# Performance work log

Measured on AMD Instinct MI355X. Metric: run time of the kernel, lower is better.

## Reference

```python
import jax, jax.numpy as jnp
import numpy as np

B, C, H, W = 2, 512, 64, 64
G = 32          # GroupNorm groups
EPS = 1e-6


def setup_inputs() -> dict:
    key = jax.random.key(0)
    ks = jax.random.split(key, 10)
    s = 1.0 / np.sqrt(C)
    return {
        "x": jax.random.normal(ks[0], (B, C, H, W), dtype=jnp.float32),
        "gn_w": jnp.ones((C,), jnp.float32),
        "gn_b": jnp.zeros((C,), jnp.float32),
        "wq": jax.random.normal(ks[1], (C, C), jnp.float32) * s,
        "bq": jnp.zeros((C,), jnp.float32),
        "wk": jax.random.normal(ks[2], (C, C), jnp.float32) * s,
        "bk": jnp.zeros((C,), jnp.float32),
        "wv": jax.random.normal(ks[3], (C, C), jnp.float32) * s,
        "bv": jnp.zeros((C,), jnp.float32),
        "wo": jax.random.normal(ks[4], (C, C), jnp.float32) * s,
        "bo": jnp.zeros((C,), jnp.float32),
    }


def reference(x, gn_w, gn_b, wq, bq, wk, bk, wv, bv, wo, bo):
    b, c, h, w = x.shape
    n = h * w
    # GroupNorm(32, eps=1e-6, affine)
    xg = x.reshape(b, G, c // G, h, w)
    mu = xg.mean(axis=(2, 3, 4), keepdims=True)
    var = ((xg - mu) ** 2).mean(axis=(2, 3, 4), keepdims=True)
    hn = ((xg - mu) * jax.lax.rsqrt(var + EPS)).reshape(b, c, h, w)
    hn = hn * gn_w[None, :, None, None] + gn_b[None, :, None, None]
    # 1x1 convs == per-pixel linear over channels; tokens: b n c
    hf = hn.reshape(b, c, n)
    q = jnp.einsum('oc,bcn->bno', wq, hf) + bq  # [b, n, c]
    k = jnp.einsum('oc,bcn->bno', wk, hf) + bk
    v = jnp.einsum('oc,bcn->bno', wv, hf) + bv
    scale = jnp.asarray(c, x.dtype) ** -0.5
    att = jax.nn.softmax(jnp.einsum('bic,bjc->bij', q, k) * scale, axis=-1)
    o = jnp.einsum('bij,bjc->bic', att, v)      # [b, n, c]
    out = jnp.einsum('oc,bnc->bno', wo, o) + bo # proj_out
    return x + out.transpose(0, 2, 1).reshape(b, c, h, w)
```

## Files before the change

kernel.cpp:

```cpp
#include <hip/hip_runtime.h>
#include <hip/hip_bf16.h>


typedef float f32x4 __attribute__((ext_vector_type(4)));
typedef __bf16 bf16x8 __attribute__((ext_vector_type(8)));

typedef const __attribute__((address_space(1))) unsigned char* gas_p;
typedef __attribute__((address_space(3))) unsigned char* las_p;

__device__ __forceinline__ void gload_lds16(const void* g, void* l) {
  __builtin_amdgcn_global_load_lds((gas_p)g, (las_p)l, 16, 0, 0);
}

__global__ __launch_bounds__(256) void prelude_k(
    const float* __restrict__ wq, const float* __restrict__ wk,
    const float* __restrict__ wv, const float* __restrict__ wo,
    __hip_bfloat16* __restrict__ wqkb, __hip_bfloat16* __restrict__ wvb,
    __hip_bfloat16* __restrict__ wob, const float* __restrict__ bq,
    const float* __restrict__ bk, float* __restrict__ bqk,
    const float* __restrict__ x, float* __restrict__ stats) {
  int bid = blockIdx.x;
  if (bid < 4096) {
    const float* src;
    __hip_bfloat16* dst;
    if (bid < 1024)      { src = wq; dst = wqkb; }
    else if (bid < 2048) { src = wk; dst = wqkb + 262144; }
    else if (bid < 3072) { src = wv; dst = wvb; }
    else                 { src = wo; dst = wob; }
    int i = (bid & 1023) * 256 + threadIdx.x;
    dst[i] = __float2bfloat16(src[i]);
    return;
  }
  if (bid < 4160) {
    int bg = bid - 4096;
    const float4* p = (const float4*)(x + (size_t)bg * 65536);
    float s = 0.f, s2 = 0.f;
    for (int i = threadIdx.x; i < 16384; i += 256) {
      float4 v = p[i];
      s  += v.x + v.y + v.z + v.w;
      s2 += v.x * v.x + v.y * v.y + v.z * v.z + v.w * v.w;
    }
#pragma unroll
    for (int off = 32; off > 0; off >>= 1) {
      s  += __shfl_xor(s, off);
      s2 += __shfl_xor(s2, off);
    }
    __shared__ float rs[4], rs2[4];
    int wid = threadIdx.x >> 6, lane = threadIdx.x & 63;
    if (lane == 0) { rs[wid] = s; rs2[wid] = s2; }
    __syncthreads();
    if (threadIdx.x == 0) {
      float S  = rs[0] + rs[1] + rs[2] + rs[3];
      float S2 = rs2[0] + rs2[1] + rs2[2] + rs2[3];
      float mean = S * (1.f / 65536.f);
      float var  = S2 * (1.f / 65536.f) - mean * mean;
      stats[bg * 2]     = mean;
      stats[bg * 2 + 1] = rsqrtf(var + 1e-6f);
    }
    return;
  }
  for (int j = threadIdx.x; j < 1024; j += 256)
    bqk[j] = (j < 512) ? bq[j] : bk[j - 512];
}

__global__ __launch_bounds__(256) void gn_apply_k(const float* __restrict__ x,
                                                  const float* __restrict__ stats,
                                                  const float* __restrict__ gw,
                                                  const float* __restrict__ gb,
                                                  __hip_bfloat16* __restrict__ hf) {
  int c0 = blockIdx.x * 64, n0 = blockIdx.y * 64, b = blockIdx.z;
  __shared__ float tile[64][65];
  int tid = threadIdx.x;
  int cl = tid >> 2, q = tid & 3;
  int c = c0 + cl;
  float mean = stats[(b * 32 + (c >> 4)) * 2];
  float rstd = stats[(b * 32 + (c >> 4)) * 2 + 1];
  float sc = rstd * gw[c];
  float sh = gb[c] - mean * sc;
  const float* xr = x + ((size_t)(b * 512 + c0 + cl)) * 4096 + n0 + q * 16;
#pragma unroll
  for (int j = 0; j < 4; j++) {
    float4 v = *(const float4*)(xr + 4 * j);
    int n = q * 16 + 4 * j;
    tile[cl][n]     = v.x * sc + sh;
    tile[cl][n + 1] = v.y * sc + sh;
    tile[cl][n + 2] = v.z * sc + sh;
    tile[cl][n + 3] = v.w * sc + sh;
  }
  __syncthreads();
  int nl = tid >> 2, ch = q * 16;
  bf16x8 o0, o1;
#pragma unroll
  for (int l = 0; l < 8; l++) {
    o0[l] = (__bf16)tile[ch + l][nl];
    o1[l] = (__bf16)tile[ch + 8 + l][nl];
  }
  __hip_bfloat16* op = hf + ((size_t)(b * 4096 + n0 + nl)) * 512 + c0 + ch;
  *(uint4*)op = *(uint4*)&o0;
  *(uint4*)(op + 8) = *(uint4*)&o1;
}

__global__ __launch_bounds__(256, 4) void qkv_k(
    const __hip_bfloat16* __restrict__ hf, const __hip_bfloat16* __restrict__ wqk,
    const __hip_bfloat16* __restrict__ wv, const float* __restrict__ bqk,
    const float* __restrict__ bv, __hip_bfloat16* __restrict__ qk,
    __hip_bfloat16* __restrict__ vT) {
  bool isV = blockIdx.x >= 8;
  int m0 = isV ? (blockIdx.x - 8) * 128 : blockIdx.y * 128;
  int n0 = isV ? blockIdx.y * 128 : blockIdx.x * 128;
  const __hip_bfloat16* A  = isV ? wv : hf;
  const __hip_bfloat16* Bm = isV ? hf : wqk;

  __shared__ __align__(16) unsigned char smem[34816];
  __hip_bfloat16* As  = (__hip_bfloat16*)smem;
  __hip_bfloat16* Bs  = As + 8192;
  __hip_bfloat16* epi = (__hip_bfloat16*)smem;

  int tid  = threadIdx.x;
  int wvx  = tid >> 6, lane = tid & 63;
  int wr   = (wvx >> 1) * 64, wc = (wvx & 1) * 64;
  int quad = lane >> 4, l16 = lane & 15;

  int srow = wvx * 32 + (lane >> 2);
  int scol = (lane & 3) * 8;
  const __hip_bfloat16* gA0 = A  + (size_t)(m0 + srow) * 512 + scol;
  const __hip_bfloat16* gA1 = gA0 + (size_t)16 * 512;
  const __hip_bfloat16* gB0 = Bm + (size_t)(n0 + srow) * 512 + scol;
  const __hip_bfloat16* gB1 = gB0 + (size_t)16 * 512;

  auto stage = [&](int kk, int bsel) {
    int lb = bsel * 4096 + wvx * 1024;
    gload_lds16(gA0 + kk, &As[lb]);
    gload_lds16(gA1 + kk, &As[lb + 512]);
    gload_lds16(gB0 + kk, &Bs[lb]);
    gload_lds16(gB1 + kk, &Bs[lb + 512]);
  };

  f32x4 acc[4][4] = {};
  stage(0, 0);
  for (int kt = 0; kt < 16; kt++) {
    __syncthreads();
    if (kt + 1 < 16) stage((kt + 1) << 5, (kt + 1) & 1);
    const __hip_bfloat16* Ab = &As[(kt & 1) * 4096];
    const __hip_bfloat16* Bb = &Bs[(kt & 1) * 4096];
    bf16x8 af[4], bfr[4];
#pragma unroll
    for (int i = 0; i < 4; i++)
      af[i] = *(const bf16x8*)&Ab[(wr + i * 16 + l16) * 32 + quad * 8];
#pragma unroll
    for (int j = 0; j < 4; j++)
      bfr[j] = *(const bf16x8*)&Bb[(wc + j * 16 + l16) * 32 + quad * 8];
#pragma unroll
    for (int i = 0; i < 4; i++)
#pragma unroll
      for (int j = 0; j < 4; j++)
        acc[i][j] = __builtin_amdgcn_mfma_f32_16x16x32_bf16(af[i], bfr[j],
                                                            acc[i][j], 0, 0, 0);
  }

  float bj[4], bm[4][4];
  if (!isV) {
#pragma unroll
    for (int j = 0; j < 4; j++) bj[j] = bqk[n0 + wc + j * 16 + l16];
  } else {
#pragma unroll
    for (int i = 0; i < 4; i++)
#pragma unroll
      for (int r = 0; r < 4; r++)
        bm[i][r] = bv[m0 + wr + i * 16 + quad * 4 + r];
  }
  __syncthreads();
#pragma unroll
  for (int i = 0; i < 4; i++)
#pragma unroll
    for (int j = 0; j < 4; j++)
#pragma unroll
      for (int r = 0; r < 4; r++) {
        int ml = wr + i * 16 + quad * 4 + r;
        int nl = wc + j * 16 + l16;
        float v = acc[i][j][r] + (isV ? bm[i][r] : bj[j]);
        epi[ml * 136 + nl] = __float2bfloat16(v);
      }
  __syncthreads();
  int mr = tid >> 1, h = tid & 1;
  const __hip_bfloat16* rowp = &epi[mr * 136 + h * 64];
  if (!isV) {
    __hip_bfloat16* o = qk + (size_t)(m0 + mr) * 1024 + n0 + h * 64;
#pragma unroll
    for (int c = 0; c < 8; c++)
      *(uint4*)(o + c * 8) = *(const uint4*)(rowp + c * 8);
  } else {
    int b = (n0 + h * 64) >> 12, t = (n0 + h * 64) & 4095;
    __hip_bfloat16* o = vT + ((size_t)(b * 512 + m0 + mr)) * 4096 + t;
#pragma unroll
    for (int c = 0; c < 8; c++)
      *(uint4*)(o + c * 8) = *(const uint4*)(rowp + c * 8);
  }
}

__global__ __launch_bounds__(512, 4) void attn_k(
    const __hip_bfloat16* __restrict__ qk, const __hip_bfloat16* __restrict__ vT,
    __hip_bfloat16* __restrict__ part, float* __restrict__ rsum) {
  const float scale = 0.044194173824159216f;
  int bid = blockIdx.x;
  int g = bid & 7;
  int b = g >> 2, spl = g & 3;
  int qtile = bid >> 3;

  const __hip_bfloat16* qkb = qk + (size_t)b * 4194304;
  const __hip_bfloat16* vTb = vT + (size_t)b * 2097152;

  __shared__ __align__(16) unsigned char smem[74752];
  __hip_bfloat16* Qs = (__hip_bfloat16*)smem;
  __hip_bfloat16* Ps = (__hip_bfloat16*)(smem + 65536);
  float* Rs = (float*)(smem + 73728);

  int tid = threadIdx.x, wv = tid >> 6, lane = tid & 63;
  int quad = lane >> 4, l16 = lane & 15;
  int kvc0 = wv * 16;

  __hip_bfloat16* slot = (__hip_bfloat16*)(smem + 32768 + wv * 4096);

#pragma unroll
  for (int i = 0; i < 4; i++) {
    int r = wv * 4 + i;
    gload_lds16(qkb + (size_t)(qtile * 32 + r) * 1024 + (lane ^ (r & 7)) * 8,
                &Qs[r * 512]);
  }

  const __hip_bfloat16* gKw =
      qkb + (size_t)(spl * 1024 + wv * 16 + (lane >> 2)) * 1024 + 512 +
      ((lane & 3) ^ ((lane >> 2) & 3)) * 8;
  auto stageK32 = [&](int t, int s) {
    gload_lds16(gKw + (size_t)t * 131072 + s * 32, slot + (s & 3) * 512);
  };

  const __hip_bfloat16* gVw =
      vTb + (size_t)(wv * 64 + (lane >> 2)) * 4096 + spl * 1024 +
      ((lane & 3) ^ ((lane >> 2) & 3)) * 8;
  auto stageVp = [&](int t, int sub) {
#pragma unroll
    for (int c = 0; c < 4; c++)
      gload_lds16(gVw + (size_t)t * 128 + sub * 32 + (size_t)(c * 16) * 4096,
                  slot + c * 512);
  };

  f32x4 accS[2] = {};
  f32x4 accO[2][4] = {};
  float rsr[8] = {};

  stageK32(0, 0);
  stageK32(0, 1);
  stageK32(0, 2);
  asm volatile("s_waitcnt vmcnt(3)" ::: "memory");
  __builtin_amdgcn_s_barrier();
  asm volatile("" ::: "memory");

  for (int t = 0; t < 8; t++) {
#pragma unroll
    for (int s = 0; s < 16; s++) {
      if (s < 13) {
        stageK32(t, s + 3);
        asm volatile("s_waitcnt vmcnt(3)" ::: "memory");
      } else if (s == 13) {
        asm volatile("s_waitcnt vmcnt(2)" ::: "memory");
      } else if (s == 14) {
        asm volatile("s_waitcnt vmcnt(1)" ::: "memory");
      } else {
        asm volatile("s_waitcnt vmcnt(0)" ::: "memory");
      }
      const __hip_bfloat16* Kb = slot + (s & 3) * 512;
      int rk = kvc0 + l16;
      (void)rk;
      bf16x8 bk = *(const bf16x8*)&Kb[l16 * 32 + ((quad ^ (l16 & 3)) << 3)];
#pragma unroll
      for (int qg = 0; qg < 2; qg++) {
        int rq = qg * 16 + l16;
        bf16x8 aq = *(const bf16x8*)
            &Qs[rq * 512 + (((s * 4 + quad) ^ (rq & 7)) << 3)];
        accS[qg] = __builtin_amdgcn_mfma_f32_16x16x32_bf16(aq, bk, accS[qg],
                                                           0, 0, 0);
      }
    }
    asm volatile("s_waitcnt lgkmcnt(0)" ::: "memory");
    stageVp(t, 0);
#pragma unroll
    for (int qg = 0; qg < 2; qg++) {
#pragma unroll
      for (int rr = 0; rr < 4; rr++) {
        float p = __expf(accS[qg][rr] * scale);
        rsr[qg * 4 + rr] += p;
        int row = qg * 16 + quad * 4 + rr;
        int col = kvc0 + l16;
        Ps[row * 128 + (((col >> 3) ^ (row & 7)) << 3) + (col & 7)] =
            __float2bfloat16(p);
      }
      accS[qg] = (f32x4){0.f, 0.f, 0.f, 0.f};
    }
    asm volatile("s_waitcnt lgkmcnt(0)" ::: "memory");
    __builtin_amdgcn_s_barrier();
    asm volatile("" ::: "memory");
#pragma unroll
    for (int sub = 0; sub < 4; sub++) {
      asm volatile("s_waitcnt vmcnt(0)" ::: "memory");
      bf16x8 pa[2], bvf[4];
#pragma unroll
      for (int qg = 0; qg < 2; qg++) {
        int rq = qg * 16 + l16;
        pa[qg] = *(const bf16x8*)
            &Ps[rq * 128 + (((sub * 4 + quad) ^ (rq & 7)) << 3)];
      }
#pragma unroll
      for (int dj = 0; dj < 4; dj++)
        bvf[dj] = *(const bf16x8*)
            &slot[(dj * 16 + l16) * 32 + ((quad ^ (l16 & 3)) << 3)];
      asm volatile("s_waitcnt lgkmcnt(0)" ::: "memory");
      __builtin_amdgcn_sched_barrier(0);
      if (sub < 3) stageVp(t, sub + 1);
#pragma unroll
      for (int dj = 0; dj < 4; dj++)
#pragma unroll
        for (int qg = 0; qg < 2; qg++)
          accO[qg][dj] = __builtin_amdgcn_mfma_f32_16x16x32_bf16(
              pa[qg], bvf[dj], accO[qg][dj], 0, 0, 0);
    }
    asm volatile("" ::: "memory");
    __builtin_amdgcn_s_barrier();
    asm volatile("" ::: "memory");
    if (t + 1 < 8) {
      stageK32(t + 1, 0);
      stageK32(t + 1, 1);
      stageK32(t + 1, 2);
    }
  }

  size_t pbase = ((size_t)(spl * 2 + b) * 4096 + qtile * 32) * 512;
#pragma unroll
  for (int qg = 0; qg < 2; qg++)
#pragma unroll
    for (int rr = 0; rr < 4; rr++) {
      int row = qg * 16 + quad * 4 + rr;
#pragma unroll
      for (int dj = 0; dj < 4; dj++)
        part[pbase + (size_t)row * 512 + wv * 64 + dj * 16 + l16] =
            __float2bfloat16(accO[qg][dj][rr]);
    }
#pragma unroll
  for (int k = 0; k < 8; k++)
#pragma unroll
    for (int off = 1; off < 16; off <<= 1) rsr[k] += __shfl_xor(rsr[k], off);
  if (l16 == 0) {
#pragma unroll
    for (int qg = 0; qg < 2; qg++)
#pragma unroll
      for (int rr = 0; rr < 4; rr++)
        Rs[wv * 32 + qg * 16 + quad * 4 + rr] = rsr[qg * 4 + rr];
  }
  __syncthreads();
  if (tid < 32) {
    float s = 0.f;
#pragma unroll
    for (int w = 0; w < 8; w++) s += Rs[w * 32 + tid];
    rsum[spl * 8192 + b * 4096 + qtile * 32 + tid] = s;
  }
}

__global__ __launch_bounds__(256) void reduce2_k(
    const __hip_bfloat16* __restrict__ part, const float* __restrict__ rsum,
    __hip_bfloat16* __restrict__ obuf) {
  size_t i8 = (size_t)blockIdx.x * 256 + threadIdx.x;
  size_t perb = 262144;
  size_t b = i8 / perb, r = i8 - b * perb;
  int t = (int)(r >> 6);
  float ps = rsum[b * 4096 + t] + rsum[8192 + b * 4096 + t] +
             rsum[16384 + b * 4096 + t] + rsum[24576 + b * 4096 + t];
  float inv = 1.f / ps;
  float acc[8] = {};
#pragma unroll
  for (int sp = 0; sp < 4; sp++) {
    bf16x8 v = ((const bf16x8*)part)[(sp * 2 + b) * perb + r];
#pragma unroll
    for (int l = 0; l < 8; l++) acc[l] += (float)v[l];
  }
  bf16x8 o;
#pragma unroll
  for (int l = 0; l < 8; l++) o[l] = (__bf16)(acc[l] * inv);
  ((bf16x8*)obuf)[b * perb + r] = o;
}

__global__ __launch_bounds__(256, 2) void oproj_k(
    const __hip_bfloat16* __restrict__ Wo, const __hip_bfloat16* __restrict__ O,
    float* __restrict__ out, const float* __restrict__ bias,
    const float* __restrict__ resid) {
  int m0 = blockIdx.y * 64, n0 = blockIdx.x * 128, bb = blockIdx.z;
  O += (size_t)bb * 4096 * 512;
  size_t cbase = (size_t)bb * 512 * 4096;

  __shared__ __align__(16) unsigned char smem[24576];
  __hip_bfloat16* As  = (__hip_bfloat16*)smem;
  __hip_bfloat16* Bs  = As + 4096;
  __hip_bfloat16* epi = (__hip_bfloat16*)smem;

  int tid = threadIdx.x, wv = tid >> 6, lane = tid & 63;
  int wr = (wv >> 1) * 32, wc = (wv & 1) * 64;
  int quad = lane >> 4, l16 = lane & 15;

  int lr = lane >> 2, scol = (lane & 3) * 8;
  const __hip_bfloat16* gA  = Wo + (size_t)(m0 + wv * 16 + lr) * 512 + scol;
  const __hip_bfloat16* gB0 = O  + (size_t)(n0 + wv * 32 + lr) * 512 + scol;
  const __hip_bfloat16* gB1 = gB0 + (size_t)16 * 512;

  auto stage = [&](int kk, int bsel) {
    gload_lds16(gA + kk, &As[bsel * 2048 + wv * 512]);
    gload_lds16(gB0 + kk, &Bs[bsel * 4096 + wv * 1024]);
    gload_lds16(gB1 + kk, &Bs[bsel * 4096 + wv * 1024 + 512]);
  };

  f32x4 acc[2][4] = {};
  stage(0, 0);
  for (int kt = 0; kt < 16; kt++) {
    __syncthreads();
    if (kt + 1 < 16) stage((kt + 1) << 5, (kt + 1) & 1);
    const __hip_bfloat16* Ab = &As[(kt & 1) * 2048];
    const __hip_bfloat16* Bb = &Bs[(kt & 1) * 4096];
    bf16x8 af[2], bfr[4];
#pragma unroll
    for (int i = 0; i < 2; i++)
      af[i] = *(const bf16x8*)&Ab[(wr + i * 16 + l16) * 32 + quad * 8];
#pragma unroll
    for (int j = 0; j < 4; j++)
      bfr[j] = *(const bf16x8*)&Bb[(wc + j * 16 + l16) * 32 + quad * 8];
#pragma unroll
    for (int i = 0; i < 2; i++)
#pragma unroll
      for (int j = 0; j < 4; j++)
        acc[i][j] = __builtin_amdgcn_mfma_f32_16x16x32_bf16(af[i], bfr[j],
                                                            acc[i][j], 0, 0, 0);
  }

  float pre[2][4];
#pragma unroll
  for (int i = 0; i < 2; i++)
#pragma unroll
    for (int r = 0; r < 4; r++)
      pre[i][r] = bias[m0 + wr + i * 16 + quad * 4 + r];
  __syncthreads();
#pragma unroll
  for (int i = 0; i < 2; i++)
#pragma unroll
    for (int j = 0; j < 4; j++)
#pragma unroll
      for (int r = 0; r < 4; r++)
        epi[(wr + i * 16 + quad * 4 + r) * 136 + wc + j * 16 + l16] =
            __float2bfloat16(acc[i][j][r] + pre[i][r]);
  __syncthreads();
  int mr = tid >> 2, seg = tid & 3;
  const __hip_bfloat16* rowp = &epi[mr * 136 + seg * 32];
  size_t obase = cbase + (size_t)(m0 + mr) * 4096 + n0 + seg * 32;
#pragma unroll
  for (int c = 0; c < 4; c++) {
    bf16x8 val = *(const bf16x8*)(rowp + c * 8);
    size_t idx = obase + c * 8;
    float4 r0 = *(const float4*)&resid[idx];
    float4 r1 = *(const float4*)&resid[idx + 4];
    float4 o0, o1;
    o0.x = r0.x + (float)val[0]; o0.y = r0.y + (float)val[1];
    o0.z = r0.z + (float)val[2]; o0.w = r0.w + (float)val[3];
    o1.x = r1.x + (float)val[4]; o1.y = r1.y + (float)val[5];
    o1.z = r1.z + (float)val[6]; o1.w = r1.w + (float)val[7];
    *(float4*)&out[idx] = o0;
    *(float4*)&out[idx + 4] = o1;
  }
}

extern "C" void kernel_launch(void* const* d_in, const int* in_sizes, int n_in,
                              void* d_out, int out_size, void* d_ws,
                              size_t ws_size, hipStream_t stream) {
  const float* xp  = (const float*)d_in[0];
  const float* gwp = (const float*)d_in[1];
  const float* gbp = (const float*)d_in[2];
  const float* wqp = (const float*)d_in[3];
  const float* bqp = (const float*)d_in[4];
  const float* wkp = (const float*)d_in[5];
  const float* bkp = (const float*)d_in[6];
  const float* wvp = (const float*)d_in[7];
  const float* bvp = (const float*)d_in[8];
  const float* wop = (const float*)d_in[9];
  const float* bop = (const float*)d_in[10];
  float* outp = (float*)d_out;

  char* w = (char*)d_ws;
  size_t off = 0;
  auto alloc = [&](size_t bytes) {
    void* p = w + off;
    off += (bytes + 255) & ~(size_t)255;
    return p;
  };
  float* stats         = (float*)alloc(64 * 2 * sizeof(float));
  __hip_bfloat16* hf   = (__hip_bfloat16*)alloc((size_t)2 * 4096 * 512 * 2);
  __hip_bfloat16* wqkb = (__hip_bfloat16*)alloc((size_t)1024 * 512 * 2);
  __hip_bfloat16* wvb  = (__hip_bfloat16*)alloc((size_t)512 * 512 * 2);
  __hip_bfloat16* wob  = (__hip_bfloat16*)alloc((size_t)512 * 512 * 2);
  float* bqk           = (float*)alloc(1024 * sizeof(float));
  float* rsum          = (float*)alloc((size_t)4 * 2 * 4096 * sizeof(float));
  __hip_bfloat16* qk   = (__hip_bfloat16*)alloc((size_t)2 * 4096 * 1024 * 2);
  __hip_bfloat16* vT   = (__hip_bfloat16*)alloc((size_t)2 * 512 * 4096 * 2);
  __hip_bfloat16* obuf = (__hip_bfloat16*)alloc((size_t)2 * 4096 * 512 * 2);
  __hip_bfloat16* part = (__hip_bfloat16*)alloc((size_t)8 * 4096 * 512 * 2);

  prelude_k<<<4161, 256, 0, stream>>>(wqp, wkp, wvp, wop, wqkb, wvb, wob,
                                      bqp, bkp, bqk, xp, stats);

  gn_apply_k<<<dim3(8, 64, 2), 256, 0, stream>>>(xp, stats, gwp, gbp, hf);

  qkv_k<<<dim3(12, 64, 1), 256, 0, stream>>>(hf, wqkb, wvb, bqk, bvp, qk, vT);

  attn_k<<<1024, 512, 0, stream>>>(qk, vT, part, rsum);

  reduce2_k<<<2048, 256, 0, stream>>>(part, rsum, obuf);

  oproj_k<<<dim3(32, 8, 2), 256, 0, stream>>>(wob, obuf, outp, bop, xp);
}
```

Baseline: 284.2 us.

## Hold Q fragments in registers, deepen K staging, double-buffer V tiles

```diff
diff --git a/kernel.cpp b/kernel.cpp
--- a/kernel.cpp
+++ b/kernel.cpp
@@ -198,7 +198,7 @@
   }
 }
 
-__global__ __launch_bounds__(512, 4) void attn_k(
+__global__ __launch_bounds__(512, 2) void attn_k(
     const __hip_bfloat16* __restrict__ qk, const __hip_bfloat16* __restrict__ vT,
     __hip_bfloat16* __restrict__ part, float* __restrict__ rsum) {
   const float scale = 0.044194173824159216f;
@@ -210,99 +210,111 @@
   const __hip_bfloat16* qkb = qk + (size_t)b * 4194304;
   const __hip_bfloat16* vTb = vT + (size_t)b * 2097152;
 
-  __shared__ __align__(16) unsigned char smem[74752];
-  __hip_bfloat16* Qs = (__hip_bfloat16*)smem;
-  __hip_bfloat16* Ps = (__hip_bfloat16*)(smem + 65536);
-  float* Rs = (float*)(smem + 73728);
+  __shared__ __align__(16) unsigned char smem[140288];
+  __hip_bfloat16* Ps = (__hip_bfloat16*)smem;
+  float* Rs = (float*)(smem + 139264);
 
   int tid = threadIdx.x, wv = tid >> 6, lane = tid & 63;
   int quad = lane >> 4, l16 = lane & 15;
   int kvc0 = wv * 16;
 
-  __hip_bfloat16* slot = (__hip_bfloat16*)(smem + 32768 + wv * 4096);
-
-#pragma unroll
-  for (int i = 0; i < 4; i++) {
-    int r = wv * 4 + i;
-    gload_lds16(qkb + (size_t)(qtile * 32 + r) * 1024 + (lane ^ (r & 7)) * 8,
-                &Qs[r * 512]);
+  __hip_bfloat16* slot = (__hip_bfloat16*)(smem + 8192 + wv * 16384);
+
+  bf16x8 qfrag[2][16];
+  {
+    const __hip_bfloat16* qrow0 =
+        qkb + (size_t)(qtile * 32 + l16) * 1024 + quad * 8;
+    const __hip_bfloat16* qrow1 = qrow0 + (size_t)16 * 1024;
+#pragma unroll
+    for (int s = 0; s < 16; s++) qfrag[0][s] = *(const bf16x8*)(qrow0 + s * 32);
+#pragma unroll
+    for (int s = 0; s < 16; s++) qfrag[1][s] = *(const bf16x8*)(qrow1 + s * 32);
   }
 
   const __hip_bfloat16* gKw =
       qkb + (size_t)(spl * 1024 + wv * 16 + (lane >> 2)) * 1024 + 512 +
       ((lane & 3) ^ ((lane >> 2) & 3)) * 8;
-  auto stageK32 = [&](int t, int s) {
-    gload_lds16(gKw + (size_t)t * 131072 + s * 32, slot + (s & 3) * 512);
+  auto stageK = [&](int t, int s) {
+    gload_lds16(gKw + (size_t)t * 131072 + s * 32, slot + s * 512);
   };
 
   const __hip_bfloat16* gVw =
       vTb + (size_t)(wv * 64 + (lane >> 2)) * 4096 + spl * 1024 +
       ((lane & 3) ^ ((lane >> 2) & 3)) * 8;
-  auto stageVp = [&](int t, int sub) {
+  auto stageV = [&](int t, int sub, int h) {
 #pragma unroll
     for (int c = 0; c < 4; c++)
       gload_lds16(gVw + (size_t)t * 128 + sub * 32 + (size_t)(c * 16) * 4096,
-                  slot + c * 512);
+                  slot + 4096 + h * 2048 + c * 512);
   };
 
   f32x4 accS[2] = {};
   f32x4 accO[2][4] = {};
-  float rsr[8] = {};
-
-  stageK32(0, 0);
-  stageK32(0, 1);
-  stageK32(0, 2);
-  asm volatile("s_waitcnt vmcnt(3)" ::: "memory");
-  __builtin_amdgcn_s_barrier();
-  asm volatile("" ::: "memory");
+  float rsr[2] = {};
+
+#pragma unroll
+  for (int p = 0; p < 8; p++) stageK(0, p);
 
   for (int t = 0; t < 8; t++) {
 #pragma unroll
     for (int s = 0; s < 16; s++) {
-      if (s < 13) {
-        stageK32(t, s + 3);
-        asm volatile("s_waitcnt vmcnt(3)" ::: "memory");
-      } else if (s == 13) {
-        asm volatile("s_waitcnt vmcnt(2)" ::: "memory");
-      } else if (s == 14) {
-        asm volatile("s_waitcnt vmcnt(1)" ::: "memory");
+      if (s < 8) {
+        stageK(t, s + 8);
+        asm volatile("s_waitcnt vmcnt(8)" ::: "memory");
+      } else if (s == 8)  asm volatile("s_waitcnt vmcnt(7)" ::: "memory");
+      else if (s == 9)  asm volatile("s_waitcnt vmcnt(6)" ::: "memory");
+      else if (s == 10) asm volatile("s_waitcnt vmcnt(5)" ::: "memory");
+      else if (s == 11) asm volatile("s_waitcnt vmcnt(4)" ::: "memory");
+      else if (s == 12) asm volatile("s_waitcnt vmcnt(3)" ::: "memory");
+      else if (s == 13) asm volatile("s_waitcnt vmcnt(2)" ::: "memory");
+      else if (s == 14) asm volatile("s_waitcnt vmcnt(1)" ::: "memory");
+      else              asm volatile("s_waitcnt vmcnt(0)" ::: "memory");
+      bf16x8 bk = *(const bf16x8*)
+          &slot[s * 512 + l16 * 32 + ((quad ^ (l16 & 3)) << 3)];
+#pragma unroll
+      for (int qg = 0; qg < 2; qg++)
+        accS[qg] = __builtin_amdgcn_mfma_f32_16x16x32_bf16(
+            bk, qfrag[qg][s], accS[qg], 0, 0, 0);
+    }
+    asm volatile("s_waitcnt lgkmcnt(0)" ::: "memory");
+    __builtin_amdgcn_sched_barrier(0);
+    stageV(t, 0, 0);
+#pragma unroll
+    for (int qg = 0; qg < 2; qg++) {
+      ushort4 pk;
+#pragma unroll
+      for (int rr = 0; rr < 4; rr++) {
+        float p = __expf(accS[qg][rr] * scale);
+        rsr[qg] += p;
+        union { __hip_bfloat16 h; unsigned short u; } cv;
+        cv.h = __float2bfloat16(p);
+        ((unsigned short*)&pk)[rr] = cv.u;
+      }
+      int q = qg * 16 + l16;
+      int chunk = (wv * 2 + (quad >> 1)) ^ (q & 7);
+      *(ushort4*)&Ps[q * 128 + chunk * 8 + (quad & 1) * 4] = pk;
+      accS[qg] = (f32x4){0.f, 0.f, 0.f, 0.f};
+    }
+    asm volatile("s_waitcnt lgkmcnt(0)" ::: "memory");
+    __builtin_amdgcn_s_barrier();
+    asm volatile("" ::: "memory");
+#pragma unroll
+    for (int sub = 0; sub < 4; sub++) {
+      if (sub > 0) {
+        asm volatile("s_waitcnt lgkmcnt(0)" ::: "memory");
+        __builtin_amdgcn_sched_barrier(0);
+      }
+      if (sub < 3) {
+        stageV(t, sub + 1, (sub + 1) & 1);
+        asm volatile("s_waitcnt vmcnt(4)" ::: "memory");
+      } else if (t + 1 < 8) {
+#pragma unroll
+        for (int p = 0; p < 8; p++) stageK(t + 1, p);
+        asm volatile("s_waitcnt vmcnt(8)" ::: "memory");
       } else {
         asm volatile("s_waitcnt vmcnt(0)" ::: "memory");
       }
-      const __hip_bfloat16* Kb = slot + (s & 3) * 512;
-      int rk = kvc0 + l16;
-      (void)rk;
-      bf16x8 bk = *(const bf16x8*)&Kb[l16 * 32 + ((quad ^ (l16 & 3)) << 3)];
-#pragma unroll
-      for (int qg = 0; qg < 2; qg++) {
-        int rq = qg * 16 + l16;
-        bf16x8 aq = *(const bf16x8*)
-            &Qs[rq * 512 + (((s * 4 + quad) ^ (rq & 7)) << 3)];
-        accS[qg] = __builtin_amdgcn_mfma_f32_16x16x32_bf16(aq, bk, accS[qg],
-                                                           0, 0, 0);
-      }
-    }
-    asm volatile("s_waitcnt lgkmcnt(0)" ::: "memory");
-    stageVp(t, 0);
-#pragma unroll
-    for (int qg = 0; qg < 2; qg++) {
-#pragma unroll
-      for (int rr = 0; rr < 4; rr++) {
-        float p = __expf(accS[qg][rr] * scale);
-        rsr[qg * 4 + rr] += p;
-        int row = qg * 16 + quad * 4 + rr;
-        int col = kvc0 + l16;
-        Ps[row * 128 + (((col >> 3) ^ (row & 7)) << 3) + (col & 7)] =
-            __float2bfloat16(p);
-      }
-      accS[qg] = (f32x4){0.f, 0.f, 0.f, 0.f};
-    }
-    asm volatile("s_waitcnt lgkmcnt(0)" ::: "memory");
-    __builtin_amdgcn_s_barrier();
-    asm volatile("" ::: "memory");
-#pragma unroll
-    for (int sub = 0; sub < 4; sub++) {
-      asm volatile("s_waitcnt vmcnt(0)" ::: "memory");
+      const __hip_bfloat16* Vb = slot + 4096 + (sub & 1) * 2048;
       bf16x8 pa[2], bvf[4];
 #pragma unroll
       for (int qg = 0; qg < 2; qg++) {
@@ -313,10 +325,7 @@
 #pragma unroll
       for (int dj = 0; dj < 4; dj++)
         bvf[dj] = *(const bf16x8*)
-            &slot[(dj * 16 + l16) * 32 + ((quad ^ (l16 & 3)) << 3)];
-      asm volatile("s_waitcnt lgkmcnt(0)" ::: "memory");
-      __builtin_amdgcn_sched_barrier(0);
-      if (sub < 3) stageVp(t, sub + 1);
+            &Vb[(dj * 16 + l16) * 32 + ((quad ^ (l16 & 3)) << 3)];
 #pragma unroll
       for (int dj = 0; dj < 4; dj++)
 #pragma unroll
@@ -324,14 +333,9 @@
           accO[qg][dj] = __builtin_amdgcn_mfma_f32_16x16x32_bf16(
               pa[qg], bvf[dj], accO[qg][dj], 0, 0, 0);
     }
-    asm volatile("" ::: "memory");
+    asm volatile("s_waitcnt lgkmcnt(0)" ::: "memory");
     __builtin_amdgcn_s_barrier();
     asm volatile("" ::: "memory");
-    if (t + 1 < 8) {
-      stageK32(t + 1, 0);
-      stageK32(t + 1, 1);
-      stageK32(t + 1, 2);
-    }
   }
 
   size_t pbase = ((size_t)(spl * 2 + b) * 4096 + qtile * 32) * 512;
@@ -346,15 +350,14 @@
             __float2bfloat16(accO[qg][dj][rr]);
     }
 #pragma unroll
-  for (int k = 0; k < 8; k++)
-#pragma unroll
-    for (int off = 1; off < 16; off <<= 1) rsr[k] += __shfl_xor(rsr[k], off);
-  if (l16 == 0) {
+  for (int qg = 0; qg < 2; qg++) {
+    rsr[qg] += __shfl_xor(rsr[qg], 16);
+    rsr[qg] += __shfl_xor(rsr[qg], 32);
+  }
+  if (quad == 0) {
 #pragma unroll
     for (int qg = 0; qg < 2; qg++)
-#pragma unroll
-      for (int rr = 0; rr < 4; rr++)
-        Rs[wv * 32 + qg * 16 + quad * 4 + rr] = rsr[qg * 4 + rr];
+      Rs[wv * 32 + qg * 16 + l16] = rsr[qg];
   }
   __syncthreads();
   if (tid < 32) {
```

New measurement: 327.4 us. 15.2% more time.
